# Performance work log

Measured on AMD Instinct MI355X. Metric: run time of the kernel, lower is better.

Reference implementation:

```python
import jax, jax.numpy as jnp
import numpy as np

B, S, E, H, ROT, MAXP = 2, 1024, 2048, 16, 64, 2048
HD = E // H
EPS = 1e-12  # torch F.normalize default eps


def _sinusoidal_positions(num_pos, dim):
    # GPT-J create_sinusoidal_positions: concat(sin, cos) along feature dim
    inv_freq = 1.0 / (10000.0 ** (np.arange(0, dim, 2, dtype=np.float32) / dim))
    sinusoid = np.einsum("i,j->ij", np.arange(num_pos, dtype=np.float32), inv_freq)
    return jnp.asarray(np.concatenate([np.sin(sinusoid), np.cos(sinusoid)], axis=-1))


def _rotate_every_two(x):
    x1 = x[..., ::2]
    x2 = x[..., 1::2]
    return jnp.stack((-x2, x1), axis=-1).reshape(x.shape)


def _apply_rotary(t, sin, cos):
    # t: [B,S,H,rot]; sin/cos: [B,S,rot/2] -> repeat_interleave(2) -> [B,S,1,rot]
    sin = jnp.repeat(sin, 2, axis=-1)[:, :, None, :]
    cos = jnp.repeat(cos, 2, axis=-1)[:, :, None, :]
    return t * cos + _rotate_every_two(t) * sin


def setup_inputs() -> dict:
    key = jax.random.key(0)
    ks = jax.random.split(key, 5)
    hidden_states = jax.random.normal(ks[0], (B, S, E), dtype=jnp.float32)
    w_q = jax.random.normal(ks[1], (E, E), dtype=jnp.float32) * 0.02
    w_k = jax.random.normal(ks[2], (E, E), dtype=jnp.float32) * 0.02
    w_v = jax.random.normal(ks[3], (E, E), dtype=jnp.float32) * 0.02
    w_o = jax.random.normal(ks[4], (E, E), dtype=jnp.float32) * 0.02
    norm_const = 0.5 * jnp.ones((1, H, 1, 1), dtype=jnp.float32)
    attention_mask = jnp.zeros((B, 1, 1, S), dtype=jnp.float32)  # 0 = attend (HF additive mask)
    position_ids = jnp.tile(jnp.arange(S, dtype=jnp.int32)[None, :], (B, 1))
    return {"hidden_states": hidden_states, "w_q": w_q, "w_k": w_k, "w_v": w_v,
            "w_o": w_o, "norm_const": norm_const, "attention_mask": attention_mask,
            "position_ids": position_ids}


def reference(hidden_states, w_q, w_k, w_v, w_o, norm_const, attention_mask, position_ids):
    b, s, e = hidden_states.shape
    # projections (nn.Linear, no bias): y = x @ W.T
    q = (hidden_states @ w_q.T).reshape(b, s, H, HD)  # rotary layout [B,S,H,hd]
    k = (hidden_states @ w_k.T).reshape(b, s, H, HD)
    v = (hidden_states @ w_v.T).reshape(b, s, H, HD).transpose(0, 2, 1, 3)  # [B,H,S,hd]

    embed = _sinusoidal_positions(MAXP, ROT)          # [MAXP, ROT]
    sincos = embed[position_ids]                      # [B,S,ROT]
    sin, cos = jnp.split(sincos, 2, axis=-1)          # each [B,S,ROT/2]

    # partial rotary on first ROT dims
    q = jnp.concatenate([_apply_rotary(q[..., :ROT], sin, cos), q[..., ROT:]], axis=-1)
    k = jnp.concatenate([_apply_rotary(k[..., :ROT], sin, cos), k[..., ROT:]], axis=-1)
    q = q.transpose(0, 2, 1, 3)  # [B,H,S,hd]
    k = k.transpose(0, 2, 1, 3)

    causal = jnp.tril(jnp.ones((s, s), dtype=bool))[None, None]   # [1,1,S,S]
    mask0 = (attention_mask == 0)                                  # [B,1,1,S] bool

    # value rescale: per-query count of visible keys ** sigmoid(norm_const), clamped >= 1
    counts = jnp.sum(causal & mask0, axis=-1, keepdims=True).astype(jnp.float32)  # [B,1,S,1]
    denom = jnp.maximum(counts ** jax.nn.sigmoid(norm_const), 1.0)                # [B,H,S,1]
    v = v / denom

    # L2-normalize q/k (torch F.normalize: x / max(||x||, eps))
    q = q / jnp.maximum(jnp.linalg.norm(q, axis=-1, keepdims=True), EPS)
    k = k / jnp.maximum(jnp.linalg.norm(k, axis=-1, keepdims=True), EPS)

    mask_t = jnp.swapaxes(mask0, -1, -2)  # [B,1,S,1]
    q = q * mask_t
    k = k * mask_t
    v = v * mask_t

    attn_weights = jnp.einsum("bhqd,bhkd->bhqk", q, k)     # cosine similarities
    attn_weights = jnp.where(causal, attn_weights, 0.0)
    attn_output = jnp.einsum("bhqk,bhkd->bhqd", attn_weights, v)

    attn_output = attn_output.transpose(0, 2, 1, 3).reshape(b, s, e)
    return attn_output @ w_o.T
```

## Files before the change

kernel.cpp:

```cpp
#include <hip/hip_runtime.h>
#include <math.h>

#define B 2
#define S 1024
#define E 2048
#define H 16
#define HD 128
#define ROT 64
#define EPSN 1e-12f

using half8 = __attribute__((ext_vector_type(8))) _Float16;
using half4 = __attribute__((ext_vector_type(4))) _Float16;
using half2 = __attribute__((ext_vector_type(2))) _Float16;
using f32x4 = __attribute__((ext_vector_type(4))) float;

__device__ __forceinline__ void gl_lds16(const void* g, void* l) {
    __builtin_amdgcn_global_load_lds(
        (const __attribute__((address_space(1))) unsigned int*)g,
        (__attribute__((address_space(3))) unsigned int*)l, 16, 0, 0);
}

#define BARX()  asm volatile("s_barrier" ::: "memory")
#define LGKM0() asm volatile("s_waitcnt lgkmcnt(0)" ::: "memory")
#define VMW(n)  asm volatile("s_waitcnt vmcnt(" #n ")" ::: "memory")

__device__ __forceinline__ int ctIdx(int row, int col) {
    int f = (row & 15) ^ ((row >> 3) & 15);
    return row * 256 + (col & 3) + (((col >> 2) ^ f) << 2);
}

__global__ __launch_bounds__(256) void prep(const float* __restrict__ x0,
                                            const float* __restrict__ x1,
                                            const float* __restrict__ x2,
                                            const float* __restrict__ x3,
                                            const float* __restrict__ x4,
                                            _Float16* __restrict__ y0,
                                            _Float16* __restrict__ y1,
                                            _Float16* __restrict__ y2,
                                            _Float16* __restrict__ y3,
                                            _Float16* __restrict__ y4,
                                            const float* __restrict__ am,
                                            const int*  __restrict__ pos,
                                            float* __restrict__ cnt,
                                            float* __restrict__ tab) {
    __shared__ float ls[256];
    const int bx = (int)blockIdx.x;
    if (bx < 20480) {
        const float* xs[5] = {x0, x1, x2, x3, x4};
        _Float16*    ys[5] = {y0, y1, y2, y3, y4};
        const int t = bx >> 12;
        const int i = (bx & 4095) * 256 + threadIdx.x;
        float4 v = ((const float4*)xs[t])[i];
        half4 h;
        h[0] = (_Float16)v.x; h[1] = (_Float16)v.y;
        h[2] = (_Float16)v.z; h[3] = (_Float16)v.w;
        ((half4*)ys[t])[i] = h;
    } else if (bx < 20736) {
        int item = (bx - 20480) * 256 + threadIdx.x;
        int bs = item >> 5, j = item & 31;
        float p = (float)pos[bs];
        float ang = p * expf(-0.28782313662425574f * (float)j);
        float s_, c_;
        sincosf(ang, &s_, &c_);
        tab[(size_t)bs * 64 + j * 2]     = c_;
        tab[(size_t)bs * 64 + j * 2 + 1] = s_;
    } else {
        const int b = bx - 20736;
        const int t = threadIdx.x;
        float v[4];
        float s4 = 0.f;
#pragma unroll
        for (int i = 0; i < 4; ++i) {
            v[i] = (am[b * S + t * 4 + i] == 0.f) ? 1.f : 0.f;
            s4 += v[i];
        }
        ls[t] = s4;
        __syncthreads();
        for (int off = 1; off < 256; off <<= 1) {
            float u = (t >= off) ? ls[t - off] : 0.f;
            __syncthreads();
            ls[t] += u;
            __syncthreads();
        }
        float run = ls[t] - s4;
#pragma unroll
        for (int i = 0; i < 4; ++i) {
            run += v[i];
            cnt[b * S + t * 4 + i] = run;
        }
    }
}

__global__ __launch_bounds__(512, 2) void gemm_qkv256(
        const _Float16* __restrict__ hs,
        const _Float16* __restrict__ wq,
        const _Float16* __restrict__ wk,
        const _Float16* __restrict__ wv,
        _Float16* __restrict__ qo,
        _Float16* __restrict__ ko,
        _Float16* __restrict__ vto,
        const float* __restrict__ am,
        const float* __restrict__ nc,
        const float* __restrict__ cnt,
        const float* __restrict__ tab) {
    __shared__ uint4 L[8][1024];
    __shared__ float sclA[256], sclB[256];

    const int lid = (int)blockIdx.x;
    const int swz = (lid & 7) * 24 + (lid >> 3);
    const int z   = swz >> 6;
    const int gm  = (swz & 63) >> 3;
    const int gn  = swz & 7;
    const _Float16* Asrc = (z == 2) ? wv : hs;
    const _Float16* Bsrc = (z == 2) ? hs : ((z == 0) ? wq : wk);
    const int mBase = gm << 8;
    const int nBase = gn << 8;

    const int tid   = (int)threadIdx.x;
    const int lane  = tid & 63;
    const int w     = tid >> 6;
    const int l15   = lane & 15;
    const int lq    = lane >> 4;
    const int wm4   = (w >> 2) << 2;
    const int wn2   = (w & 3) << 1;
    const int wbase = tid & 448;

    if (tid < 256) {
        if (z == 2) {
            const int bbv  = nBase >> 10;
            const int sgx  = (nBase & (S - 1)) + tid;
            const int h0v  = mBase >> 7;
            float valid = (am[bbv * S + sgx] == 0.f) ? 1.f : 0.f;
            float c  = cnt[bbv * S + sgx];
            float g0 = 1.f / (1.f + expf(-nc[h0v]));
            float g1 = 1.f / (1.f + expf(-nc[h0v + 1]));
            sclA[tid] = valid / fmaxf(powf(c, g0), 1.f);
            sclB[tid] = valid / fmaxf(powf(c, g1), 1.f);
        } else {
            const int bb  = mBase >> 10;
            const int sgx = (mBase & (S - 1)) + tid;
            sclA[tid] = (am[bb * S + sgx] == 0.f) ? 1.f : 0.f;
        }
    }

    f32x4 acc[2][2][4][2];
#pragma unroll
    for (int X = 0; X < 2; ++X)
#pragma unroll
        for (int Y = 0; Y < 2; ++Y)
#pragma unroll
            for (int mt = 0; mt < 4; ++mt)
#pragma unroll
                for (int nt = 0; nt < 2; ++nt)
                    acc[X][Y][mt][nt] = (f32x4){0.f, 0.f, 0.f, 0.f};

    half8 af[4][2], wf[2][2];

    auto stage = [&](int slot, const _Float16* src, int rowBase, int hf, int kt) {
#pragma unroll
        for (int j = 0; j < 2; ++j) {
            const int c  = (j << 9) + tid;
            const int rb = c >> 7;
            const int q  = (c >> 4) & 7;
            const int r  = c & 15;
            gl_lds16(&src[(size_t)(rowBase + hf * 128 + rb * 16 + r) * E +
                          kt * 64 + q * 8],
                     &L[slot][(j << 9) + wbase]);
        }
    };
    auto ldsA = [&](int db, int X) {
#pragma unroll
        for (int mt = 0; mt < 4; ++mt)
#pragma unroll
            for (int ks = 0; ks < 2; ++ks)
                af[mt][ks] = *(const half8*)&L[db * 2 + X]
                    [(wm4 + mt) * 128 + (ks * 4 + lq) * 16 + l15];
    };
    auto ldsB = [&](int db, int Y) {
#pragma unroll
        for (int nt = 0; nt < 2; ++nt)
#pragma unroll
            for (int ks = 0; ks < 2; ++ks)
                wf[nt][ks] = *(const half8*)&L[4 + db * 2 + Y]
                    [(wn2 + nt) * 128 + (ks * 4 + lq) * 16 + l15];
    };
    auto mma = [&](int X, int Y) {
        __builtin_amdgcn_s_setprio(1);
#pragma unroll
        for (int mt = 0; mt < 4; ++mt)
#pragma unroll
            for (int nt = 0; nt < 2; ++nt)
#pragma unroll
                for (int ks = 0; ks < 2; ++ks)
                    acc[X][Y][mt][nt] = __builtin_amdgcn_mfma_f32_16x16x32_f16(
                        af[mt][ks], wf[nt][ks], acc[X][Y][mt][nt], 0, 0, 0);
        __builtin_amdgcn_s_setprio(0);
    };

    stage(0, Asrc, mBase, 0, 0);
    stage(4, Bsrc, nBase, 0, 0);
    stage(1, Asrc, mBase, 1, 0);
    stage(5, Bsrc, nBase, 1, 0);
    stage(2, Asrc, mBase, 0, 1);
    stage(7, Bsrc, nBase, 1, 1);
    stage(3, Asrc, mBase, 1, 1);
    VMW(6);
    BARX();

    for (int j = 0; j < 16; ++j) {
        const int tB  = 2 * j + 1;
        const int tN0 = 2 * j + 2;
        const int tN1 = 2 * j + 3;
        const bool more = (j < 15);

        ldsA(0, 0); ldsB(0, 0);
        stage(6, Bsrc, nBase, 0, tB);
        BARX(); LGKM0();
        mma(0, 0);
        BARX();

        ldsB(0, 1);
        if (more) stage(0, Asrc, mBase, 0, tN0);
        BARX(); LGKM0();
        mma(0, 1);
        BARX();

        ldsA(0, 1);
        if (more) stage(5, Bsrc, nBase, 1, tN0);
        BARX(); LGKM0();
        mma(1, 1);
        BARX();

        ldsB(0, 0);
        if (more) { stage(1, Asrc, mBase, 1, tN0); VMW(4); }
        else      { VMW(0); }
        BARX(); LGKM0();
        mma(1, 0);
        BARX();

        ldsA(1, 0); ldsB(1, 0);
        if (more) stage(4, Bsrc, nBase, 0, tN0);
        BARX(); LGKM0();
        mma(0, 0);
        BARX();

        ldsB(1, 1);
        if (more) stage(2, Asrc, mBase, 0, tN1);
        BARX(); LGKM0();
        mma(0, 1);
        BARX();

        ldsA(1, 1);
        if (more) stage(7, Bsrc, nBase, 1, tN1);
        BARX(); LGKM0();
        mma(1, 1);
        BARX();

        ldsB(1, 0);
        if (more) stage(3, Asrc, mBase, 1, tN1);
        VMW(4);
        BARX(); LGKM0();
        mma(1, 0);
        BARX();
    }

    if (z < 2) {
        const int bb  = mBase >> 10;
        const int sB0 = mBase & (S - 1);
        const int h0  = nBase >> 7;
        VMW(0);
        BARX();
        _Float16* CtH = (_Float16*)&L[0][0];
#pragma unroll
        for (int X = 0; X < 2; ++X)
#pragma unroll
            for (int Y = 0; Y < 2; ++Y)
#pragma unroll
                for (int mt = 0; mt < 4; ++mt)
#pragma unroll
                    for (int nt = 0; nt < 2; ++nt)
#pragma unroll
                        for (int r = 0; r < 4; ++r) {
                            int row = X * 128 + (w >> 2) * 64 + mt * 16 + lq * 4 + r;
                            int col = Y * 128 + (w & 3) * 32 + nt * 16 + l15;
                            CtH[ctIdx(row, col)] = (_Float16)acc[X][Y][mt][nt][r];
                        }
        __syncthreads();

        const int row = tid >> 1;
        const int hh  = tid & 1;
        const int sg  = sB0 + row;
        const float* tb = &tab[((size_t)bb * S + sg) * 64];

        half4 gv[32];
        float ss = 0.f;
#pragma unroll
        for (int k = 0; k < 32; ++k) {
            half4 x = *(const half4*)&CtH[ctIdx(row, hh * 128 + k * 4)];
            float v0 = x[0], v1 = x[1], v2 = x[2], v3 = x[3];
            if (k < 16) {
                float4 t4 = *(const float4*)&tb[k * 4];
                float t0 = v0 * t4.x - v1 * t4.y;
                float t1 = v1 * t4.x + v0 * t4.y;
                float t2 = v2 * t4.z - v3 * t4.w;
                float t3 = v3 * t4.z + v2 * t4.w;
                v0 = t0; v1 = t1; v2 = t2; v3 = t3;
            }
            ss += v0 * v0 + v1 * v1 + v2 * v2 + v3 * v3;
            half4 y;
            y[0] = (_Float16)v0; y[1] = (_Float16)v1;
            y[2] = (_Float16)v2; y[3] = (_Float16)v3;
            gv[k] = y;
        }
        float scl = sclA[row] / fmaxf(sqrtf(ss), EPSN);
        _Float16* rowOut = (z == 0) ? qo : ko;
        _Float16* gp = &rowOut[(((size_t)bb * H + h0 + hh) * S + sg) * HD];
#pragma unroll
        for (int k = 0; k < 32; ++k) {
            half4 y;
            y[0] = (_Float16)((float)gv[k][0] * scl);
            y[1] = (_Float16)((float)gv[k][1] * scl);
            y[2] = (_Float16)((float)gv[k][2] * scl);
            y[3] = (_Float16)((float)gv[k][3] * scl);
            *(half4*)&gp[k * 4] = y;
        }
    } else {
        const int bbv  = nBase >> 10;
        const int sB0v = nBase & (S - 1);
        const int h0v  = mBase >> 7;
#pragma unroll
        for (int X = 0; X < 2; ++X)
#pragma unroll
            for (int Y = 0; Y < 2; ++Y)
#pragma unroll
                for (int mt = 0; mt < 4; ++mt)
#pragma unroll
                    for (int nt = 0; nt < 2; ++nt)
#pragma unroll
                        for (int r = 0; r < 4; ++r) {
                            int dvRow = X * 128 + (w >> 2) * 64 + mt * 16 + lq * 4 + r;
                            int sCol  = Y * 128 + (w & 3) * 32 + nt * 16 + l15;
                            float scl = X ? sclB[sCol] : sclA[sCol];
                            vto[((size_t)(bbv * H + h0v + X) * HD + (dvRow & 127)) * S +
                                sB0v + sCol] =
                                (_Float16)(acc[X][Y][mt][nt][r] * scl);
                        }
    }
}

__global__ __launch_bounds__(256) void kvp(const _Float16* __restrict__ kh,
                                           const _Float16* __restrict__ vt,
                                           _Float16* __restrict__ ut) {
    __shared__ _Float16 Kt_s[HD][72];
    __shared__ _Float16 Vt_s[32][72];
    const int slice = blockIdx.x;
    const int bh    = blockIdx.y;
    const int tid = threadIdx.x;
    const int lane = tid & 63, w = tid >> 6;
    const int l15 = lane & 15, lq = lane >> 4;
    const size_t kbase = (size_t)bh * S * HD;
    const size_t vbase = ((size_t)bh * HD + slice * 32) * S;

    f32x4 accr[2][2];
#pragma unroll
    for (int mt = 0; mt < 2; ++mt)
#pragma unroll
        for (int nt = 0; nt < 2; ++nt)
            accr[mt][nt] = (f32x4){0.f, 0.f, 0.f, 0.f};

    for (int c = 0; c < 16; ++c) {
        const int c0 = c * 64;
        half8 kreg[4];
#pragma unroll
        for (int j = 0; j < 4; ++j)
            kreg[j] = *(const half8*)&kh[kbase + (size_t)(c0 + lane) * HD +
                                         (j * 4 + w) * 8];
        uint4 vreg = *(const uint4*)&vt[vbase + (size_t)(tid >> 3) * S +
                                        c0 + (tid & 7) * 8];

        const size_t ub = ((size_t)bh * 16 + c) << 14;
#pragma unroll
        for (int mt = 0; mt < 2; ++mt)
#pragma unroll
            for (int nt = 0; nt < 2; ++nt) {
                int mtg = w * 2 + mt, ntg = slice * 2 + nt;
                int f0 = ntg * 2048 + (mtg >> 1) * 512 +
                         (l15 + ((mtg * 2 + (lq >> 1)) & 3) * 16) * 8 +
                         (lq & 1) * 4;
                half4 hv;
                hv[0] = (_Float16)accr[mt][nt][0];
                hv[1] = (_Float16)accr[mt][nt][1];
                hv[2] = (_Float16)accr[mt][nt][2];
                hv[3] = (_Float16)accr[mt][nt][3];
                *(half4*)&ut[ub + f0] = hv;
            }

        __syncthreads();
#pragma unroll
        for (int j = 0; j < 4; ++j)
#pragma unroll
            for (int i = 0; i < 8; ++i)
                Kt_s[(j * 4 + w) * 8 + i][lane] = kreg[j][i];
        *(uint4*)&Vt_s[tid >> 3][(tid & 7) * 8] = vreg;
        __syncthreads();

#pragma unroll
        for (int ks = 0; ks < 2; ++ks) {
            half8 afv[2], wfv[2];
#pragma unroll
            for (int mt = 0; mt < 2; ++mt)
                afv[mt] = *(const half8*)&Kt_s[(w * 2 + mt) * 16 + l15]
                                              [ks * 32 + lq * 8];
#pragma unroll
            for (int nt = 0; nt < 2; ++nt)
                wfv[nt] = *(const half8*)&Vt_s[nt * 16 + l15][ks * 32 + lq * 8];
#pragma unroll
            for (int mt = 0; mt < 2; ++mt)
#pragma unroll
                for (int nt = 0; nt < 2; ++nt)
                    accr[mt][nt] = __builtin_amdgcn_mfma_f32_16x16x32_f16(
                        afv[mt], wfv[nt], accr[mt][nt], 0, 0, 0);
        }
    }
}

__global__ __launch_bounds__(256) void attn_local(const _Float16* __restrict__ qh,
                                                  const _Float16* __restrict__ kh,
                                                  const _Float16* __restrict__ vt,
                                                  const _Float16* __restrict__ mt,
                                                  _Float16* __restrict__ o) {
    __shared__ _Float16 Ks[64][136];
    __shared__ _Float16 Vs[HD][72];
    __shared__ _Float16 Ps[64][72];
    __shared__ uint4 Ms[2048];

    const int qt = blockIdx.x;
    const int bh = blockIdx.y;
    const int b = bh >> 4, h = bh & 15;
    const int tid = threadIdx.x;
    const int lane = tid & 63;
    const int w = tid >> 6;
    const int l15 = lane & 15;
    const int lq = lane >> 4;
    const int qBase = qt * 64;
    const size_t sd_base = (size_t)bh * S * HD;

    half8 qf[4];
#pragma unroll
    for (int ks = 0; ks < 4; ++ks)
        qf[ks] = *(const half8*)&qh[sd_base + (size_t)(qBase + w * 16 + l15) * HD +
                                    ks * 32 + lq * 8];

    const _Float16* mtc = mt + (((size_t)bh * 16 + qt) << 14);
#pragma unroll
    for (int rr = 0; rr < 8; ++rr)
        gl_lds16(&mtc[(size_t)((rr * 4 + w) * 64 + lane) * 8],
                 &Ms[(rr * 4 + w) * 64]);

    uint4 pk[4], pv[4];
#pragma unroll
    for (int j = 0; j < 4; ++j) {
        int f = tid + j * 256;
        int rK = f >> 4, c8K = f & 15;
        int rV = f >> 3, c8V = f & 7;
        pk[j] = *(const uint4*)&kh[sd_base + (size_t)(qBase + rK) * HD + c8K * 8];
        pv[j] = *(const uint4*)&vt[sd_base + (size_t)rV * S + qBase + c8V * 8];
    }
#pragma unroll
    for (int j = 0; j < 4; ++j) {
        int f = tid + j * 256;
        int rK = f >> 4, c8K = f & 15;
        int rV = f >> 3, c8V = f & 7;
        *(uint4*)&Ks[rK][c8K * 8] = pk[j];
        *(uint4*)&Vs[rV][c8V * 8] = pv[j];
    }
    __syncthreads();

    f32x4 sacc[4];
#pragma unroll
    for (int nt = 0; nt < 4; ++nt)
        sacc[nt] = (f32x4){0.f, 0.f, 0.f, 0.f};
#pragma unroll
    for (int nt = 0; nt < 4; ++nt)
#pragma unroll
        for (int ks = 0; ks < 4; ++ks) {
            half8 kf = *(const half8*)&Ks[nt * 16 + l15][ks * 32 + lq * 8];
            sacc[nt] = __builtin_amdgcn_mfma_f32_16x16x32_f16(qf[ks], kf,
                                                              sacc[nt], 0, 0, 0);
        }

#pragma unroll
    for (int nt = 0; nt < 4; ++nt)
#pragma unroll
        for (int r = 0; r < 4; ++r) {
            int ql = w * 16 + lq * 4 + r;
            int kl = nt * 16 + l15;
            float sv = (kl <= ql) ? sacc[nt][r] : 0.f;
            Ps[ql][kl] = (_Float16)sv;
        }

    f32x4 oacc[8];
#pragma unroll
    for (int dt = 0; dt < 8; ++dt)
        oacc[dt] = (f32x4){0.f, 0.f, 0.f, 0.f};
#pragma unroll
    for (int dt = 0; dt < 8; ++dt)
#pragma unroll
        for (int km = 0; km < 4; ++km) {
            half8 mf = *(const half8*)&Ms[(dt * 4 + km) * 64 + lane];
            oacc[dt] = __builtin_amdgcn_mfma_f32_16x16x32_f16(qf[km], mf,
                                                              oacc[dt], 0, 0, 0);
        }
    __syncthreads();

    half8 pf[2];
    pf[0] = *(const half8*)&Ps[w * 16 + l15][lq * 8];
    pf[1] = *(const half8*)&Ps[w * 16 + l15][32 + lq * 8];
#pragma unroll
    for (int dt = 0; dt < 8; ++dt)
#pragma unroll
        for (int ks = 0; ks < 2; ++ks) {
            half8 vf = *(const half8*)&Vs[dt * 16 + l15][ks * 32 + lq * 8];
            oacc[dt] = __builtin_amdgcn_mfma_f32_16x16x32_f16(pf[ks], vf,
                                                              oacc[dt], 0, 0, 0);
        }

#pragma unroll
    for (int dt = 0; dt < 8; ++dt)
#pragma unroll
        for (int r = 0; r < 4; ++r)
            Ks[w * 16 + lq * 4 + r][dt * 16 + l15] = (_Float16)oacc[dt][r];
    __syncthreads();
#pragma unroll
    for (int j = 0; j < 4; ++j) {
        int f = tid + j * 256;
        int ql = f >> 4, c8 = f & 15;
        *(uint4*)&o[(size_t)(b * S + qBase + ql) * E + h * HD + c8 * 8] =
            *(const uint4*)&Ks[ql][c8 * 8];
    }
}

__global__ __launch_bounds__(256) void gemm_out(const _Float16* __restrict__ A,
                                                const _Float16* __restrict__ Wp,
                                                float* __restrict__ C) {
    __shared__ uint4 As_l[2][512];
    __shared__ uint4 Ws_l[2][512];
    const int lid = (int)blockIdx.x;
    const int swz = (lid & 7) * 32 + (lid >> 3);
    const int gm  = swz >> 4;
    const int gn  = swz & 15;
    const int tid  = threadIdx.x;
    const int lane = tid & 63;
    const int w    = tid >> 6;
    const int wm   = (w >> 1) * 64;
    const int wn   = (w & 1) * 64;
    const int l15  = lane & 15;
    const int lq   = lane >> 4;
    const int r16  = lane & 15;
    const int kq4  = lane >> 4;
    const int mBase = gm * 128;
    const int nBase = gn * 128;

    f32x4 acc[4][4];
#pragma unroll
    for (int mt = 0; mt < 4; ++mt)
#pragma unroll
        for (int nt = 0; nt < 4; ++nt)
            acc[mt][nt] = (f32x4){0.f, 0.f, 0.f, 0.f};

    auto stage = [&](int bf, int k0) {
#pragma unroll
        for (int i = 0; i < 2; ++i) {
            int rb = w * 2 + i;
            gl_lds16(&A[(size_t)(mBase + rb * 16 + r16) * E + k0 + kq4 * 8],
                     &As_l[bf][rb * 64]);
            gl_lds16(&Wp[(size_t)(nBase + rb * 16 + r16) * E + k0 + kq4 * 8],
                     &Ws_l[bf][rb * 64]);
        }
    };

    stage(0, 0);
    const int nIter = E / 32;
    for (int it = 0; it < nIter; ++it) {
        __syncthreads();
        if (it + 1 < nIter) stage((it + 1) & 1, (it + 1) * 32);

        const int cur = it & 1;
        half8 af[4], wfr[4];
#pragma unroll
        for (int t = 0; t < 4; ++t) {
            int rbA = (wm >> 4) + t;
            int rbW = (wn >> 4) + t;
            af[t]  = *(const half8*)&As_l[cur][rbA * 64 + lq * 16 + l15];
            wfr[t] = *(const half8*)&Ws_l[cur][rbW * 64 + lq * 16 + l15];
        }
#pragma unroll
        for (int mt = 0; mt < 4; ++mt)
#pragma unroll
            for (int nt = 0; nt < 4; ++nt)
                acc[mt][nt] = __builtin_amdgcn_mfma_f32_16x16x32_f16(
                    af[mt], wfr[nt], acc[mt][nt], 0, 0, 0);
    }

#pragma unroll
    for (int mt = 0; mt < 4; ++mt)
#pragma unroll
        for (int nt = 0; nt < 4; ++nt)
#pragma unroll
            for (int r = 0; r < 4; ++r) {
                int row = mBase + wm + mt * 16 + lq * 4 + r;
                int col = nBase + wn + nt * 16 + l15;
                C[(size_t)row * E + col] = acc[mt][nt][r];
            }
}

extern "C" void kernel_launch(void* const* d_in, const int* in_sizes, int n_in,
                              void* d_out, int out_size, void* d_ws, size_t ws_size,
                              hipStream_t stream) {
    (void)in_sizes; (void)n_in; (void)out_size; (void)ws_size;
    const float* hs = (const float*)d_in[0];
    const float* wq = (const float*)d_in[1];
    const float* wk = (const float*)d_in[2];
    const float* wv = (const float*)d_in[3];
    const float* wo = (const float*)d_in[4];
    const float* nc = (const float*)d_in[5];
    const float* am = (const float*)d_in[6];
    const int*  pos = (const int*)d_in[7];
    float* out = (float*)d_out;

    const size_t act = (size_t)B * S * E;
    _Float16* hsb = (_Float16*)d_ws;
    _Float16* wqb = hsb + act;
    _Float16* wkb = wqb + act;
    _Float16* wvb = wkb + act;
    _Float16* wob = wvb + act;
    _Float16* qhh = wob + act;
    _Float16* khh = qhh + act;
    _Float16* vtt = khh + act;
    _Float16* abb = vtt + act;
    _Float16* utm = wqb;
    float*    cnt = (float*)abb;
    float*    tab = cnt + B * S;

    prep<<<20480 + 256 + B, 256, 0, stream>>>(
        hs, wq, wk, wv, wo, hsb, wqb, wkb, wvb, wob, am, pos, cnt, tab);

    gemm_qkv256<<<192, 512, 0, stream>>>(hsb, wqb, wkb, wvb,
                                         qhh, khh, vtt, am, nc, cnt, tab);

    kvp<<<dim3(4, B * H), 256, 0, stream>>>(khh, vtt, utm);

    attn_local<<<dim3(16, B * H), 256, 0, stream>>>(qhh, khh, vtt, utm, abb);

    gemm_out<<<256, 256, 0, stream>>>(abb, wob, out);
}
```

Baseline: 295.1 us.

## Fuse kvp, attention and output GEMM into one cooperative kernel with grid syncs

Replaces the three tail kernels (KV prefix products, local attention, output projection) with a single cooperative kernel of 256 blocks that runs each phase and separates them with grid.sync(). This removes two kernel launch gaps and their tails, at the cost of a larger shared allocation and fixed grid sizing (kvp work is split into more, thinner slices and attention runs two units per block). The QKV GEMM's V-transpose epilogue is also changed to stage through LDS and write 16-byte vectors instead of scattered 2-byte stores.

```diff
diff --git a/kernel.cpp b/kernel.cpp
--- a/kernel.cpp
+++ b/kernel.cpp
@@ -1,5 +1,8 @@
 #include <hip/hip_runtime.h>
+#include <hip/hip_cooperative_groups.h>
 #include <math.h>
+
+namespace cg = cooperative_groups;
 
 #define B 2
 #define S 1024
@@ -328,6 +331,9 @@
         const int bbv  = nBase >> 10;
         const int sB0v = nBase & (S - 1);
         const int h0v  = mBase >> 7;
+        VMW(0);
+        BARX();
+        _Float16* CtH = (_Float16*)&L[0][0];
 #pragma unroll
         for (int X = 0; X < 2; ++X)
 #pragma unroll
@@ -338,280 +344,287 @@
                     for (int nt = 0; nt < 2; ++nt)
 #pragma unroll
                         for (int r = 0; r < 4; ++r) {
-                            int dvRow = X * 128 + (w >> 2) * 64 + mt * 16 + lq * 4 + r;
-                            int sCol  = Y * 128 + (w & 3) * 32 + nt * 16 + l15;
-                            float scl = X ? sclB[sCol] : sclA[sCol];
-                            vto[((size_t)(bbv * H + h0v + X) * HD + (dvRow & 127)) * S +
-                                sB0v + sCol] =
+                            int row = X * 128 + (w >> 2) * 64 + mt * 16 + lq * 4 + r;
+                            int col = Y * 128 + (w & 3) * 32 + nt * 16 + l15;
+                            float scl = X ? sclB[col] : sclA[col];
+                            CtH[ctIdx(row, col)] =
                                 (_Float16)(acc[X][Y][mt][nt][r] * scl);
                         }
+        __syncthreads();
+#pragma unroll
+        for (int i = 0; i < 16; ++i) {
+            int f  = tid + i * 512;
+            int dr = f >> 5;
+            int sc = f & 31;
+            half4 a = *(const half4*)&CtH[ctIdx(dr, sc * 8)];
+            half4 b = *(const half4*)&CtH[ctIdx(dr, sc * 8 + 4)];
+            half8 hv;
+            hv[0] = a[0]; hv[1] = a[1]; hv[2] = a[2]; hv[3] = a[3];
+            hv[4] = b[0]; hv[5] = b[1]; hv[6] = b[2]; hv[7] = b[3];
+            *(half8*)&vto[((size_t)(bbv * H + h0v + (dr >> 7)) * HD +
+                           (dr & 127)) * S + sB0v + sc * 8] = hv;
+        }
     }
 }
 
-__global__ __launch_bounds__(256) void kvp(const _Float16* __restrict__ kh,
-                                           const _Float16* __restrict__ vt,
-                                           _Float16* __restrict__ ut) {
-    __shared__ _Float16 Kt_s[HD][72];
-    __shared__ _Float16 Vt_s[32][72];
-    const int slice = blockIdx.x;
-    const int bh    = blockIdx.y;
-    const int tid = threadIdx.x;
+__global__ __launch_bounds__(256) void tail(const _Float16* __restrict__ kh,
+                                            const _Float16* __restrict__ vt,
+                                            _Float16* __restrict__ ut,
+                                            const _Float16* __restrict__ qh,
+                                            _Float16* __restrict__ abb,
+                                            const _Float16* __restrict__ wob,
+                                            float* __restrict__ out) {
+    __shared__ __align__(16) unsigned char SMEM[77824];
+    cg::grid_group grid = cg::this_grid();
+    const int bx = (int)blockIdx.x;
+    const int tid = (int)threadIdx.x;
     const int lane = tid & 63, w = tid >> 6;
     const int l15 = lane & 15, lq = lane >> 4;
-    const size_t kbase = (size_t)bh * S * HD;
-    const size_t vbase = ((size_t)bh * HD + slice * 32) * S;
-
-    f32x4 accr[2][2];
-#pragma unroll
-    for (int mt = 0; mt < 2; ++mt)
-#pragma unroll
-        for (int nt = 0; nt < 2; ++nt)
-            accr[mt][nt] = (f32x4){0.f, 0.f, 0.f, 0.f};
-
-    for (int c = 0; c < 16; ++c) {
-        const int c0 = c * 64;
-        half8 kreg[4];
-#pragma unroll
-        for (int j = 0; j < 4; ++j)
-            kreg[j] = *(const half8*)&kh[kbase + (size_t)(c0 + lane) * HD +
-                                         (j * 4 + w) * 8];
-        uint4 vreg = *(const uint4*)&vt[vbase + (size_t)(tid >> 3) * S +
-                                        c0 + (tid & 7) * 8];
-
-        const size_t ub = ((size_t)bh * 16 + c) << 14;
-#pragma unroll
-        for (int mt = 0; mt < 2; ++mt)
-#pragma unroll
-            for (int nt = 0; nt < 2; ++nt) {
-                int mtg = w * 2 + mt, ntg = slice * 2 + nt;
-                int f0 = ntg * 2048 + (mtg >> 1) * 512 +
+
+    {
+        _Float16 (*Kt_s)[72] = (_Float16(*)[72])SMEM;
+        _Float16 (*Vt_s)[72] = (_Float16(*)[72])(SMEM + 18432);
+        const int slice = bx & 7;
+        const int bh    = bx >> 3;
+        const size_t kbase = (size_t)bh * S * HD;
+        const size_t vbase = ((size_t)bh * HD + slice * 16) * S;
+
+        f32x4 accr[2];
+        accr[0] = (f32x4){0.f, 0.f, 0.f, 0.f};
+        accr[1] = (f32x4){0.f, 0.f, 0.f, 0.f};
+
+        for (int c = 0; c < 16; ++c) {
+            const int c0 = c * 64;
+            half8 kreg[4];
+#pragma unroll
+            for (int j = 0; j < 4; ++j)
+                kreg[j] = *(const half8*)&kh[kbase + (size_t)(c0 + lane) * HD +
+                                             (j * 4 + w) * 8];
+            uint4 vreg = {0, 0, 0, 0};
+            if (tid < 128)
+                vreg = *(const uint4*)&vt[vbase + (size_t)(tid >> 3) * S +
+                                          c0 + (tid & 7) * 8];
+
+            const size_t ub = ((size_t)bh * 16 + c) << 14;
+#pragma unroll
+            for (int mt = 0; mt < 2; ++mt) {
+                int mtg = w * 2 + mt;
+                int f0 = slice * 2048 + (mtg >> 1) * 512 +
                          (l15 + ((mtg * 2 + (lq >> 1)) & 3) * 16) * 8 +
                          (lq & 1) * 4;
                 half4 hv;
-                hv[0] = (_Float16)accr[mt][nt][0];
-                hv[1] = (_Float16)accr[mt][nt][1];
-                hv[2] = (_Float16)accr[mt][nt][2];
-                hv[3] = (_Float16)accr[mt][nt][3];
+                hv[0] = (_Float16)accr[mt][0];
+                hv[1] = (_Float16)accr[mt][1];
+                hv[2] = (_Float16)accr[mt][2];
+                hv[3] = (_Float16)accr[mt][3];
                 *(half4*)&ut[ub + f0] = hv;
             }
 
-        __syncthreads();
-#pragma unroll
-        for (int j = 0; j < 4; ++j)
-#pragma unroll
-            for (int i = 0; i < 8; ++i)
-                Kt_s[(j * 4 + w) * 8 + i][lane] = kreg[j][i];
-        *(uint4*)&Vt_s[tid >> 3][(tid & 7) * 8] = vreg;
-        __syncthreads();
-
-#pragma unroll
-        for (int ks = 0; ks < 2; ++ks) {
-            half8 afv[2], wfv[2];
-#pragma unroll
-            for (int mt = 0; mt < 2; ++mt)
-                afv[mt] = *(const half8*)&Kt_s[(w * 2 + mt) * 16 + l15]
-                                              [ks * 32 + lq * 8];
-#pragma unroll
-            for (int nt = 0; nt < 2; ++nt)
-                wfv[nt] = *(const half8*)&Vt_s[nt * 16 + l15][ks * 32 + lq * 8];
-#pragma unroll
-            for (int mt = 0; mt < 2; ++mt)
-#pragma unroll
-                for (int nt = 0; nt < 2; ++nt)
-                    accr[mt][nt] = __builtin_amdgcn_mfma_f32_16x16x32_f16(
-                        afv[mt], wfv[nt], accr[mt][nt], 0, 0, 0);
+            __syncthreads();
+#pragma unroll
+            for (int j = 0; j < 4; ++j)
+#pragma unroll
+                for (int i = 0; i < 8; ++i)
+                    Kt_s[(j * 4 + w) * 8 + i][lane] = kreg[j][i];
+            if (tid < 128)
+                *(uint4*)&Vt_s[tid >> 3][(tid & 7) * 8] = vreg;
+            __syncthreads();
+
+#pragma unroll
+            for (int ks = 0; ks < 2; ++ks) {
+                half8 afv[2], wfv;
+#pragma unroll
+                for (int mt = 0; mt < 2; ++mt)
+                    afv[mt] = *(const half8*)&Kt_s[(w * 2 + mt) * 16 + l15]
+                                                  [ks * 32 + lq * 8];
+                wfv = *(const half8*)&Vt_s[l15][ks * 32 + lq * 8];
+#pragma unroll
+                for (int mt = 0; mt < 2; ++mt)
+                    accr[mt] = __builtin_amdgcn_mfma_f32_16x16x32_f16(
+                        afv[mt], wfv, accr[mt], 0, 0, 0);
+            }
         }
     }
-}
-
-__global__ __launch_bounds__(256) void attn_local(const _Float16* __restrict__ qh,
-                                                  const _Float16* __restrict__ kh,
-                                                  const _Float16* __restrict__ vt,
-                                                  const _Float16* __restrict__ mt,
-                                                  _Float16* __restrict__ o) {
-    __shared__ _Float16 Ks[64][136];
-    __shared__ _Float16 Vs[HD][72];
-    __shared__ _Float16 Ps[64][72];
-    __shared__ uint4 Ms[2048];
-
-    const int qt = blockIdx.x;
-    const int bh = blockIdx.y;
-    const int b = bh >> 4, h = bh & 15;
-    const int tid = threadIdx.x;
-    const int lane = tid & 63;
-    const int w = tid >> 6;
-    const int l15 = lane & 15;
-    const int lq = lane >> 4;
-    const int qBase = qt * 64;
-    const size_t sd_base = (size_t)bh * S * HD;
-
-    half8 qf[4];
-#pragma unroll
-    for (int ks = 0; ks < 4; ++ks)
-        qf[ks] = *(const half8*)&qh[sd_base + (size_t)(qBase + w * 16 + l15) * HD +
-                                    ks * 32 + lq * 8];
-
-    const _Float16* mtc = mt + (((size_t)bh * 16 + qt) << 14);
-#pragma unroll
-    for (int rr = 0; rr < 8; ++rr)
-        gl_lds16(&mtc[(size_t)((rr * 4 + w) * 64 + lane) * 8],
-                 &Ms[(rr * 4 + w) * 64]);
-
-    uint4 pk[4], pv[4];
-#pragma unroll
-    for (int j = 0; j < 4; ++j) {
-        int f = tid + j * 256;
-        int rK = f >> 4, c8K = f & 15;
-        int rV = f >> 3, c8V = f & 7;
-        pk[j] = *(const uint4*)&kh[sd_base + (size_t)(qBase + rK) * HD + c8K * 8];
-        pv[j] = *(const uint4*)&vt[sd_base + (size_t)rV * S + qBase + c8V * 8];
+    grid.sync();
+
+    {
+        _Float16 (*Ks)[136] = (_Float16(*)[136])SMEM;
+        _Float16 (*Vs)[72]  = (_Float16(*)[72])(SMEM + 17408);
+        _Float16 (*Ps)[72]  = (_Float16(*)[72])(SMEM + 35840);
+        uint4*    Ms        = (uint4*)(SMEM + 45056);
+
+        for (int u = 0; u < 2; ++u) {
+            const int unit = bx + u * 256;
+            const int qt = unit & 15;
+            const int bh = unit >> 4;
+            const int b = bh >> 4, h = bh & 15;
+            const int qBase = qt * 64;
+            const size_t sd_base = (size_t)bh * S * HD;
+
+            half8 qf[4];
+#pragma unroll
+            for (int ks = 0; ks < 4; ++ks)
+                qf[ks] = *(const half8*)&qh[sd_base +
+                                            (size_t)(qBase + w * 16 + l15) * HD +
+                                            ks * 32 + lq * 8];
+
+            const _Float16* mtc = ut + (((size_t)bh * 16 + qt) << 14);
+#pragma unroll
+            for (int rr = 0; rr < 8; ++rr)
+                gl_lds16(&mtc[(size_t)((rr * 4 + w) * 64 + lane) * 8],
+                         &Ms[(rr * 4 + w) * 64]);
+
+            uint4 pk[4], pv[4];
+#pragma unroll
+            for (int j = 0; j < 4; ++j) {
+                int f = tid + j * 256;
+                int rK = f >> 4, c8K = f & 15;
+                int rV = f >> 3, c8V = f & 7;
+                pk[j] = *(const uint4*)&kh[sd_base + (size_t)(qBase + rK) * HD +
+                                           c8K * 8];
+                pv[j] = *(const uint4*)&vt[sd_base + (size_t)rV * S + qBase +
+                                           c8V * 8];
+            }
+#pragma unroll
+            for (int j = 0; j < 4; ++j) {
+                int f = tid + j * 256;
+                int rK = f >> 4, c8K = f & 15;
+                int rV = f >> 3, c8V = f & 7;
+                *(uint4*)&Ks[rK][c8K * 8] = pk[j];
+                *(uint4*)&Vs[rV][c8V * 8] = pv[j];
+            }
+            __syncthreads();
+
+            f32x4 sacc[4];
+#pragma unroll
+            for (int nt = 0; nt < 4; ++nt)
+                sacc[nt] = (f32x4){0.f, 0.f, 0.f, 0.f};
+#pragma unroll
+            for (int nt = 0; nt < 4; ++nt)
+#pragma unroll
+                for (int ks = 0; ks < 4; ++ks) {
+                    half8 kf = *(const half8*)&Ks[nt * 16 + l15][ks * 32 + lq * 8];
+                    sacc[nt] = __builtin_amdgcn_mfma_f32_16x16x32_f16(
+                        qf[ks], kf, sacc[nt], 0, 0, 0);
+                }
+
+#pragma unroll
+            for (int nt = 0; nt < 4; ++nt)
+#pragma unroll
+                for (int r = 0; r < 4; ++r) {
+                    int ql = w * 16 + lq * 4 + r;
+                    int kl = nt * 16 + l15;
+                    float sv = (kl <= ql) ? sacc[nt][r] : 0.f;
+                    Ps[ql][kl] = (_Float16)sv;
+                }
+
+            f32x4 oacc[8];
+#pragma unroll
+            for (int dt = 0; dt < 8; ++dt)
+                oacc[dt] = (f32x4){0.f, 0.f, 0.f, 0.f};
+#pragma unroll
+            for (int dt = 0; dt < 8; ++dt)
+#pragma unroll
+                for (int km = 0; km < 4; ++km) {
+                    half8 mf = *(const half8*)&Ms[(dt * 4 + km) * 64 + lane];
+                    oacc[dt] = __builtin_amdgcn_mfma_f32_16x16x32_f16(
+                        qf[km], mf, oacc[dt], 0, 0, 0);
+                }
+            __syncthreads();
+
+            half8 pf[2];
+            pf[0] = *(const half8*)&Ps[w * 16 + l15][lq * 8];
+            pf[1] = *(const half8*)&Ps[w * 16 + l15][32 + lq * 8];
+#pragma unroll
+            for (int dt = 0; dt < 8; ++dt)
+#pragma unroll
+                for (int ks = 0; ks < 2; ++ks) {
+                    half8 vf = *(const half8*)&Vs[dt * 16 + l15][ks * 32 + lq * 8];
+                    oacc[dt] = __builtin_amdgcn_mfma_f32_16x16x32_f16(
+                        pf[ks], vf, oacc[dt], 0, 0, 0);
+                }
+
+#pragma unroll
+            for (int dt = 0; dt < 8; ++dt)
+#pragma unroll
+                for (int r = 0; r < 4; ++r)
+                    Ks[w * 16 + lq * 4 + r][dt * 16 + l15] = (_Float16)oacc[dt][r];
+            __syncthreads();
+#pragma unroll
+            for (int j = 0; j < 4; ++j) {
+                int f = tid + j * 256;
+                int ql = f >> 4, c8 = f & 15;
+                *(uint4*)&abb[(size_t)(b * S + qBase + ql) * E + h * HD + c8 * 8] =
+                    *(const uint4*)&Ks[ql][c8 * 8];
+            }
+            __syncthreads();
+        }
     }
-#pragma unroll
-    for (int j = 0; j < 4; ++j) {
-        int f = tid + j * 256;
-        int rK = f >> 4, c8K = f & 15;
-        int rV = f >> 3, c8V = f & 7;
-        *(uint4*)&Ks[rK][c8K * 8] = pk[j];
-        *(uint4*)&Vs[rV][c8V * 8] = pv[j];
+    grid.sync();
+
+    {
+        uint4 (*As_l)[512] = (uint4(*)[512])SMEM;
+        uint4 (*Ws_l)[512] = (uint4(*)[512])(SMEM + 16384);
+        const int swz = (bx & 7) * 32 + (bx >> 3);
+        const int gm  = swz >> 4;
+        const int gn  = swz & 15;
+        const int wm   = (w >> 1) * 64;
+        const int wn   = (w & 1) * 64;
+        const int mBase = gm * 128;
+        const int nBase = gn * 128;
+
+        f32x4 acc[4][4];
+#pragma unroll
+        for (int mt = 0; mt < 4; ++mt)
+#pragma unroll
+            for (int nt = 0; nt < 4; ++nt)
+                acc[mt][nt] = (f32x4){0.f, 0.f, 0.f, 0.f};
+
+        auto stage = [&](int bf, int k0) {
+#pragma unroll
+            for (int i = 0; i < 2; ++i) {
+                int rb = w * 2 + i;
+                gl_lds16(&abb[(size_t)(mBase + rb * 16 + l15) * E + k0 + lq * 8],
+                         &As_l[bf][rb * 64]);
+                gl_lds16(&wob[(size_t)(nBase + rb * 16 + l15) * E + k0 + lq * 8],
+                         &Ws_l[bf][rb * 64]);
+            }
+        };
+
+        stage(0, 0);
+        const int nIter = E / 32;
+        for (int it = 0; it < nIter; ++it) {
+            __syncthreads();
+            if (it + 1 < nIter) stage((it + 1) & 1, (it + 1) * 32);
+
+            const int cur = it & 1;
+            half8 af[4], wfr[4];
+#pragma unroll
+            for (int t = 0; t < 4; ++t) {
+                int rbA = (wm >> 4) + t;
+                int rbW = (wn >> 4) + t;
+                af[t]  = *(const half8*)&As_l[cur][rbA * 64 + lq * 16 + l15];
+                wfr[t] = *(const half8*)&Ws_l[cur][rbW * 64 + lq * 16 + l15];
+            }
+#pragma unroll
+            for (int mt = 0; mt < 4; ++mt)
+#pragma unroll
+                for (int nt = 0; nt < 4; ++nt)
+                    acc[mt][nt] = __builtin_amdgcn_mfma_f32_16x16x32_f16(
+                        af[mt], wfr[nt], acc[mt][nt], 0, 0, 0);
+        }
+
+#pragma unroll
+        for (int mt = 0; mt < 4; ++mt)
+#pragma unroll
+            for (int nt = 0; nt < 4; ++nt)
+#pragma unroll
+                for (int r = 0; r < 4; ++r) {
+                    int row = mBase + wm + mt * 16 + lq * 4 + r;
+                    int col = nBase + wn + nt * 16 + l15;
+                    out[(size_t)row * E + col] = acc[mt][nt][r];
+                }
     }
-    __syncthreads();
-
-    f32x4 sacc[4];
-#pragma unroll
-    for (int nt = 0; nt < 4; ++nt)
-        sacc[nt] = (f32x4){0.f, 0.f, 0.f, 0.f};
-#pragma unroll
-    for (int nt = 0; nt < 4; ++nt)
-#pragma unroll
-        for (int ks = 0; ks < 4; ++ks) {
-            half8 kf = *(const half8*)&Ks[nt * 16 + l15][ks * 32 + lq * 8];
-            sacc[nt] = __builtin_amdgcn_mfma_f32_16x16x32_f16(qf[ks], kf,
-                                                              sacc[nt], 0, 0, 0);
-        }
-
-#pragma unroll
-    for (int nt = 0; nt < 4; ++nt)
-#pragma unroll
-        for (int r = 0; r < 4; ++r) {
-            int ql = w * 16 + lq * 4 + r;
-            int kl = nt * 16 + l15;
-            float sv = (kl <= ql) ? sacc[nt][r] : 0.f;
-            Ps[ql][kl] = (_Float16)sv;
-        }
-
-    f32x4 oacc[8];
-#pragma unroll
-    for (int dt = 0; dt < 8; ++dt)
-        oacc[dt] = (f32x4){0.f, 0.f, 0.f, 0.f};
-#pragma unroll
-    for (int dt = 0; dt < 8; ++dt)
-#pragma unroll
-        for (int km = 0; km < 4; ++km) {
-            half8 mf = *(const half8*)&Ms[(dt * 4 + km) * 64 + lane];
-            oacc[dt] = __builtin_amdgcn_mfma_f32_16x16x32_f16(qf[km], mf,
-                                                              oacc[dt], 0, 0, 0);
-        }
-    __syncthreads();
-
-    half8 pf[2];
-    pf[0] = *(const half8*)&Ps[w * 16 + l15][lq * 8];
-    pf[1] = *(const half8*)&Ps[w * 16 + l15][32 + lq * 8];
-#pragma unroll
-    for (int dt = 0; dt < 8; ++dt)
-#pragma unroll
-        for (int ks = 0; ks < 2; ++ks) {
-            half8 vf = *(const half8*)&Vs[dt * 16 + l15][ks * 32 + lq * 8];
-            oacc[dt] = __builtin_amdgcn_mfma_f32_16x16x32_f16(pf[ks], vf,
-                                                              oacc[dt], 0, 0, 0);
-        }
-
-#pragma unroll
-    for (int dt = 0; dt < 8; ++dt)
-#pragma unroll
-        for (int r = 0; r < 4; ++r)
-            Ks[w * 16 + lq * 4 + r][dt * 16 + l15] = (_Float16)oacc[dt][r];
-    __syncthreads();
-#pragma unroll
-    for (int j = 0; j < 4; ++j) {
-        int f = tid + j * 256;
-        int ql = f >> 4, c8 = f & 15;
-        *(uint4*)&o[(size_t)(b * S + qBase + ql) * E + h * HD + c8 * 8] =
-            *(const uint4*)&Ks[ql][c8 * 8];
-    }
-}
-
-__global__ __launch_bounds__(256) void gemm_out(const _Float16* __restrict__ A,
-                                                const _Float16* __restrict__ Wp,
-                                                float* __restrict__ C) {
-    __shared__ uint4 As_l[2][512];
-    __shared__ uint4 Ws_l[2][512];
-    const int lid = (int)blockIdx.x;
-    const int swz = (lid & 7) * 32 + (lid >> 3);
-    const int gm  = swz >> 4;
-    const int gn  = swz & 15;
-    const int tid  = threadIdx.x;
-    const int lane = tid & 63;
-    const int w    = tid >> 6;
-    const int wm   = (w >> 1) * 64;
-    const int wn   = (w & 1) * 64;
-    const int l15  = lane & 15;
-    const int lq   = lane >> 4;
-    const int r16  = lane & 15;
-    const int kq4  = lane >> 4;
-    const int mBase = gm * 128;
-    const int nBase = gn * 128;
-
-    f32x4 acc[4][4];
-#pragma unroll
-    for (int mt = 0; mt < 4; ++mt)
-#pragma unroll
-        for (int nt = 0; nt < 4; ++nt)
-            acc[mt][nt] = (f32x4){0.f, 0.f, 0.f, 0.f};
-
-    auto stage = [&](int bf, int k0) {
-#pragma unroll
-        for (int i = 0; i < 2; ++i) {
-            int rb = w * 2 + i;
-            gl_lds16(&A[(size_t)(mBase + rb * 16 + r16) * E + k0 + kq4 * 8],
-                     &As_l[bf][rb * 64]);
-            gl_lds16(&Wp[(size_t)(nBase + rb * 16 + r16) * E + k0 + kq4 * 8],
-                     &Ws_l[bf][rb * 64]);
-        }
-    };
-
-    stage(0, 0);
-    const int nIter = E / 32;
-    for (int it = 0; it < nIter; ++it) {
-        __syncthreads();
-        if (it + 1 < nIter) stage((it + 1) & 1, (it + 1) * 32);
-
-        const int cur = it & 1;
-        half8 af[4], wfr[4];
-#pragma unroll
-        for (int t = 0; t < 4; ++t) {
-            int rbA = (wm >> 4) + t;
-            int rbW = (wn >> 4) + t;
-            af[t]  = *(const half8*)&As_l[cur][rbA * 64 + lq * 16 + l15];
-            wfr[t] = *(const half8*)&Ws_l[cur][rbW * 64 + lq * 16 + l15];
-        }
-#pragma unroll
-        for (int mt = 0; mt < 4; ++mt)
-#pragma unroll
-            for (int nt = 0; nt < 4; ++nt)
-                acc[mt][nt] = __builtin_amdgcn_mfma_f32_16x16x32_f16(
-                    af[mt], wfr[nt], acc[mt][nt], 0, 0, 0);
-    }
-
-#pragma unroll
-    for (int mt = 0; mt < 4; ++mt)
-#pragma unroll
-        for (int nt = 0; nt < 4; ++nt)
-#pragma unroll
-            for (int r = 0; r < 4; ++r) {
-                int row = mBase + wm + mt * 16 + lq * 4 + r;
-                int col = nBase + wn + nt * 16 + l15;
-                C[(size_t)row * E + col] = acc[mt][nt][r];
-            }
 }
 
 extern "C" void kernel_launch(void* const* d_in, const int* in_sizes, int n_in,
@@ -648,9 +661,8 @@
     gemm_qkv256<<<192, 512, 0, stream>>>(hsb, wqb, wkb, wvb,
                                          qhh, khh, vtt, am, nc, cnt, tab);
 
-    kvp<<<dim3(4, B * H), 256, 0, stream>>>(khh, vtt, utm);
-
-    attn_local<<<dim3(16, B * H), 256, 0, stream>>>(qhh, khh, vtt, utm, abb);
-
-    gemm_out<<<256, 256, 0, stream>>>(abb, wob, out);
+    void* targs[] = {(void*)&khh, (void*)&vtt, (void*)&utm, (void*)&qhh,
+                     (void*)&abb, (void*)&wob, (void*)&out};
+    hipLaunchCooperativeKernel((const void*)tail, dim3(256), dim3(256),
+                               targs, 0, stream);
 }
```

New measurement: 351.7 us. 1.19x slower.
